# Kernel tuning notes

Hardware: AMD Instinct MI355X
Metric: run time of the kernel (lower is better)

The kernel has to match this reference:

```python
import jax, jax.numpy as jnp
import numpy as np

STEPS = 200
H = 0.5
N_POP = 100000.0
CLAMP = 100000.0
BATCH = 65536


def setup_inputs() -> dict:
    key = jax.random.key(0)
    k1, k2 = jax.random.split(key)
    # init state [B, 1, 4] = (S, E, I, R); positive values
    init = jax.random.uniform(k1, (BATCH, 1, 4), dtype=jnp.float32) * 1000.0
    # weights mirrors nn.Parameter([100000, 3, 6, 0, 0.5, 0.2, 0.25]) with small noise
    base = jnp.array([100000.0, 3.0, 6.0, 0.0, 0.5, 0.2, 0.25], dtype=jnp.float32)
    weights = base + 0.01 * jax.random.normal(k2, (7,), dtype=jnp.float32)
    return {"init": init, "weights": weights}


def reference(init, weights):
    A, B, C = weights[4], weights[5], weights[6]

    def step(x, _):
        # x: [B, 1, 4]
        s, e, i = x[:, 0, 0], x[:, 0, 1], x[:, 0, 2]
        infl = B * s * (e + i) / N_POP
        d = jnp.stack((-infl, infl - A * e, A * e - C * i, C * i), axis=-1)  # [B, 4]
        x_new = x + H * jnp.clip(d[:, None, :], -CLAMP, CLAMP)  # [B, 1, 4]
        return x_new, x_new

    _, outs = jax.lax.scan(step, init, None, length=STEPS)  # [steps, B, 1, 4]
    return jnp.moveaxis(outs, 0, 1)  # [B, steps, 1, 4]
```

## Files before the change

### kernel.cpp

```cpp
#include <hip/hip_runtime.h>

#define BATCH 65536
#define STEPS 200
#define NPOP 100000.0f
#define CLAMP_V 100000.0f
#define H_STEP 0.5f

__global__ __launch_bounds__(256) void seir_kernel(
    const float* __restrict__ init,
    const float* __restrict__ w,
    float* __restrict__ out)
{
    const int b = blockIdx.x * blockDim.x + threadIdx.x;
    if (b >= BATCH) return;

    const float A = w[4];
    const float B = w[5];
    const float C = w[6];
    const float invN = 1.0f / NPOP;

    float4 x = reinterpret_cast<const float4*>(init)[b];
    float4* o = reinterpret_cast<float4*>(out) + (size_t)b * STEPS;

    #pragma unroll 4
    for (int t = 0; t < STEPS; ++t) {
        float infl = B * x.x * (x.y + x.z) * invN;
        float ae = A * x.y;
        float ci = C * x.z;
        float d0 = -infl;
        float d1 = infl - ae;
        float d2 = ae - ci;
        float d3 = ci;
        d0 = fminf(fmaxf(d0, -CLAMP_V), CLAMP_V);
        d1 = fminf(fmaxf(d1, -CLAMP_V), CLAMP_V);
        d2 = fminf(fmaxf(d2, -CLAMP_V), CLAMP_V);
        d3 = fminf(fmaxf(d3, -CLAMP_V), CLAMP_V);
        x.x += H_STEP * d0;
        x.y += H_STEP * d1;
        x.z += H_STEP * d2;
        x.w += H_STEP * d3;
        o[t] = x;
    }
}

extern "C" void kernel_launch(void* const* d_in, const int* in_sizes, int n_in,
                              void* d_out, int out_size, void* d_ws, size_t ws_size,
                              hipStream_t stream) {
    const float* init = (const float*)d_in[0];
    const float* w    = (const float*)d_in[1];
    float* out        = (float*)d_out;

    seir_kernel<<<dim3(BATCH / 256), dim3(256), 0, stream>>>(init, w, out);
}
```

Before: 229.8 us.

## Stage timestep chunks in LDS to coalesce output stores

Each thread writes 8 timesteps of state into shared memory, then the block cooperatively writes them out so consecutive lanes write contiguous 128-byte runs per batch row. This targets the strided per-thread float4 stores of the original. It adds two barriers per chunk and LDS traffic, and shrinks blocks to 64 threads, which lowers occupancy.

```diff
diff --git a/kernel.cpp b/kernel.cpp
--- a/kernel.cpp
+++ b/kernel.cpp
@@ -1,45 +1,68 @@
 #include <hip/hip_runtime.h>
 
-#define BATCH 65536
-#define STEPS 200
-#define NPOP 100000.0f
-#define CLAMP_V 100000.0f
-#define H_STEP 0.5f
+#define BATCH   65536
+#define STEPS   200
+#define TCHUNK  8
+#define NCHUNK  (STEPS / TCHUNK)
+#define BLK     64
+#define LSTRIDE 33
 
-__global__ __launch_bounds__(256) void seir_kernel(
+__global__ __launch_bounds__(BLK) void seir_kernel(
     const float* __restrict__ init,
     const float* __restrict__ w,
     float* __restrict__ out)
 {
-    const int b = blockIdx.x * blockDim.x + threadIdx.x;
-    if (b >= BATCH) return;
+    __shared__ float lds[BLK * LSTRIDE];
+
+    const int lane   = threadIdx.x;
+    const int base_b = blockIdx.x * BLK;
+    const int b      = base_b + lane;
 
     const float A = w[4];
     const float B = w[5];
     const float C = w[6];
-    const float invN = 1.0f / NPOP;
+    const float invN = 1.0f / 100000.0f;
 
     float4 x = reinterpret_cast<const float4*>(init)[b];
-    float4* o = reinterpret_cast<float4*>(out) + (size_t)b * STEPS;
+    float4* outf4 = reinterpret_cast<float4*>(out);
 
-    #pragma unroll 4
-    for (int t = 0; t < STEPS; ++t) {
-        float infl = B * x.x * (x.y + x.z) * invN;
-        float ae = A * x.y;
-        float ci = C * x.z;
-        float d0 = -infl;
-        float d1 = infl - ae;
-        float d2 = ae - ci;
-        float d3 = ci;
-        d0 = fminf(fmaxf(d0, -CLAMP_V), CLAMP_V);
-        d1 = fminf(fmaxf(d1, -CLAMP_V), CLAMP_V);
-        d2 = fminf(fmaxf(d2, -CLAMP_V), CLAMP_V);
-        d3 = fminf(fmaxf(d3, -CLAMP_V), CLAMP_V);
-        x.x += H_STEP * d0;
-        x.y += H_STEP * d1;
-        x.z += H_STEP * d2;
-        x.w += H_STEP * d3;
-        o[t] = x;
+    for (int chunk = 0; chunk < NCHUNK; ++chunk) {
+        #pragma unroll
+        for (int tt = 0; tt < TCHUNK; ++tt) {
+            float infl = B * x.x * (x.y + x.z) * invN;
+            float ae = A * x.y;
+            float ci = C * x.z;
+            float d0 = -infl;
+            float d1 = infl - ae;
+            float d2 = ae - ci;
+            float d3 = ci;
+            d0 = fminf(fmaxf(d0, -100000.0f), 100000.0f);
+            d1 = fminf(fmaxf(d1, -100000.0f), 100000.0f);
+            d2 = fminf(fmaxf(d2, -100000.0f), 100000.0f);
+            d3 = fminf(fmaxf(d3, -100000.0f), 100000.0f);
+            x.x += 0.5f * d0;
+            x.y += 0.5f * d1;
+            x.z += 0.5f * d2;
+            x.w += 0.5f * d3;
+            const int a = lane * LSTRIDE + tt * 4;
+            lds[a + 0] = x.x;
+            lds[a + 1] = x.y;
+            lds[a + 2] = x.z;
+            lds[a + 3] = x.w;
+        }
+        __syncthreads();
+
+        const int t0 = chunk * TCHUNK;
+        #pragma unroll
+        for (int k = 0; k < 8; ++k) {
+            const int s  = k * BLK + lane;
+            const int bb = s >> 3;
+            const int j  = s & 7;
+            const int a  = bb * LSTRIDE + j * 4;
+            float4 v = make_float4(lds[a + 0], lds[a + 1], lds[a + 2], lds[a + 3]);
+            outf4[(size_t)(base_b + bb) * STEPS + t0 + j] = v;
+        }
+        __syncthreads();
     }
 }
 
@@ -50,5 +73,5 @@
     const float* w    = (const float*)d_in[1];
     float* out        = (float*)d_out;
 
-    seir_kernel<<<dim3(BATCH / 256), dim3(256), 0, stream>>>(init, w, out);
+    seir_kernel<<<dim3(BATCH / BLK), dim3(BLK), 0, stream>>>(init, w, out);
 }
```

Result: faster. 204.7 us (-10.9%).
